# Kernel tuning notes

Hardware: AMD Instinct MI355X
Metric: run time of the kernel (lower is better)

Reference implementation:

```python
import jax, jax.numpy as jnp
import numpy as np

N_NODES = 10000
N_EDGES = 320000
D = 128
H = 4
C = 128
L = 2
NEG_SLOPE = 0.2
LN_EPS = 1e-5


def setup_inputs() -> dict:
    key = jax.random.key(0)
    ks = jax.random.split(key, 8)
    x = jax.random.normal(ks[0], (N_NODES, D), dtype=jnp.float32)
    edge_index = jax.random.randint(ks[1], (2, N_EDGES), 0, N_NODES, dtype=jnp.int64)
    # weights scaled ~Glorot to keep attention logits in a sane range
    Wl = jax.random.normal(ks[2], (L, D, H * C), dtype=jnp.float32) * 0.1
    Wr = jax.random.normal(ks[3], (L, D, H * C), dtype=jnp.float32) * 0.1
    att = jax.random.normal(ks[4], (L, H, C), dtype=jnp.float32) * 0.1
    return {
        "x": x,
        "edge_index": edge_index,
        "Wl": Wl,
        "bl": jnp.zeros((L, H * C), jnp.float32),
        "Wr": Wr,
        "br": jnp.zeros((L, H * C), jnp.float32),
        "att": att,
        "bias": jnp.zeros((L, D), jnp.float32),
        "ln_g": jnp.ones((L, D), jnp.float32),
        "ln_b": jnp.zeros((L, D), jnp.float32),
    }


def _gatv2_layer(x, src, dst, Wl, bl, Wr, br, att, b):
    """GATv2Conv (concat=False -> head mean), messages src->dst, softmax over dst."""
    n = x.shape[0]
    xl = (x @ Wl + bl).reshape(n, H, C)  # source transform
    xr = (x @ Wr + br).reshape(n, H, C)  # target transform
    s = jax.nn.leaky_relu(xl[src] + xr[dst], NEG_SLOPE)  # [E, H, C]
    e = jnp.einsum("ehc,hc->eh", s, att)  # attention logits [E, H]
    m = jax.ops.segment_max(e, dst, num_segments=n)  # stable softmax per dst segment
    ex = jnp.exp(e - m[dst])
    denom = jax.ops.segment_sum(ex, dst, num_segments=n)
    alpha = ex / denom[dst]  # [E, H]
    out = jax.ops.segment_sum(alpha[:, :, None] * xl[src], dst, num_segments=n)  # [N, H, C]
    return out.mean(axis=1) + b  # concat=False -> mean over heads, then bias


def _layer_norm(h, g, b):
    mu = h.mean(-1, keepdims=True)
    var = ((h - mu) ** 2).mean(-1, keepdims=True)
    return (h - mu) * jax.lax.rsqrt(var + LN_EPS) * g + b


def reference(x, edge_index, Wl, bl, Wr, br, att, bias, ln_g, ln_b):
    n = x.shape[0]
    loop = jnp.arange(n, dtype=edge_index.dtype)
    src = jnp.concatenate([edge_index[0], loop])  # add self-loops (PyG default)
    dst = jnp.concatenate([edge_index[1], loop])
    for i in range(L):
        h = _gatv2_layer(x, src, dst, Wl[i], bl[i], Wr[i], br[i], att[i], bias[i])
        x = h + x  # residual
        x = jax.nn.relu(_layer_norm(x, ln_g[i], ln_b[i]))
    return x
```

## Files before the change

kernel.cpp:

```cpp
#include <hip/hip_runtime.h>
#include <math.h>

#define N_NODES 10000
#define N_EDGES 320000
#define E_TOT   (N_EDGES + N_NODES)
#define NEG 0.2f
#define CAP 96

typedef short bf16x8 __attribute__((ext_vector_type(8)));
typedef float f32x4 __attribute__((ext_vector_type(4)));
typedef float f32x2 __attribute__((ext_vector_type(2)));

static __device__ __forceinline__ float4 ld4g(const float* p) { return *(const float4*)p; }

static __device__ __forceinline__ uint4 ldg4(const unsigned short* p, unsigned byteoff) {
    return *(const uint4*)((const char*)p + byteoff);
}

static __device__ __forceinline__ unsigned short f2b(float f) {
    unsigned u;
    __builtin_memcpy(&u, &f, 4);
    unsigned r = (u + 0x7fffu + ((u >> 16) & 1u)) >> 16;
    return (unsigned short)r;
}
static __device__ __forceinline__ f32x2 unpk(unsigned d) {
    f32x2 r;
    r.x = __uint_as_float(d << 16);
    r.y = __uint_as_float(d & 0xffff0000u);
    return r;
}

template <int CTRL>
static __device__ __forceinline__ float dpp_add_step(float x) {
    int y = __builtin_amdgcn_update_dpp(0, __float_as_int(x), CTRL, 0xf, 0xf, true);
    return x + __int_as_float(y);
}
static __device__ __forceinline__ float row_sum16(float x) {
    x = dpp_add_step<0x121>(x);
    x = dpp_add_step<0x122>(x);
    x = dpp_add_step<0x124>(x);
    x = dpp_add_step<0x128>(x);
    return x;
}

__global__ __launch_bounds__(256) void prep_fused_kernel(
    const float* __restrict__ x,
    const float* __restrict__ Wl, const float* __restrict__ Wr,
    unsigned short* __restrict__ xb, unsigned short* __restrict__ WT,
    int* __restrict__ deg) {
    int tid = threadIdx.x, bid = blockIdx.x;
    __shared__ float tbuf[32][33];

    for (int i = bid * 256 + tid; i < N_NODES; i += 256 * 256) deg[i] = 0;

    int l = bid >> 7;
    int rest = bid & 127;
    int ky = rest >> 5, nx = rest & 31;
    int n0 = nx * 32, k0 = ky * 32;
    const float* S = ((n0 < 512) ? Wl : Wr) + (size_t)l * 65536;
    int nn0 = n0 & 511;
    int tx = tid & 31, ty = tid >> 5;
#pragma unroll
    for (int it = 0; it < 4; ++it) {
        int k = k0 + ty + it * 8;
        tbuf[ty + it * 8][tx] = S[(size_t)k * 512 + nn0 + tx];
    }
    __syncthreads();
    unsigned short* dstp = WT + (size_t)l * 1024 * 128;
#pragma unroll
    for (int it = 0; it < 4; ++it) {
        int n = n0 + ty + it * 8;
        int k = k0 + tx;
        dstp[(size_t)n * 128 + k] = f2b(tbuf[tx][ty + it * 8]);
    }
    for (int i = bid * 256 + tid; i < N_NODES * 32; i += 256 * 256) {
        float4 v = ld4g(x + 4 * i);
        ushort4 o = make_ushort4(f2b(v.x), f2b(v.y), f2b(v.z), f2b(v.w));
        *(ushort4*)(xb + 4 * i) = o;
    }
}

template <int DO_FILL>
__global__ __launch_bounds__(256) void gemm_mfma_kernel(const unsigned short* __restrict__ A,
                                                        const unsigned short* __restrict__ Bt,
                                                        const float* __restrict__ bl,
                                                        const float* __restrict__ br,
                                                        unsigned short* __restrict__ Y,
                                                        const int* __restrict__ ei,
                                                        int* __restrict__ deg,
                                                        int* __restrict__ csr_src) {
    __shared__ unsigned short As[128][72];
    __shared__ unsigned short Bs[128][72];
    int tid = threadIdx.x;
    int wave = tid >> 6, lane = tid & 63;
    int wm = wave >> 1, wn = wave & 1;
    int l15 = lane & 15, quad = lane >> 4;
    int row0 = blockIdx.y * 128, col0 = blockIdx.x * 128;
    const float* bias = (col0 < 512) ? (bl + col0) : (br + col0 - 512);

    f32x4 acc[4][4];
#pragma unroll
    for (int mi = 0; mi < 4; ++mi)
#pragma unroll
        for (int ni = 0; ni < 4; ++ni)
#pragma unroll
            for (int r = 0; r < 4; ++r) acc[mi][ni][r] = 0.f;

#pragma unroll
    for (int kc = 0; kc < 2; ++kc) {
#pragma unroll
        for (int it = 0; it < 4; ++it) {
            int e = tid + it * 256;
            int r = e >> 3, s = e & 7;
            int gr = row0 + r;
            bf16x8 v = (bf16x8)(short)0;
            if (gr < N_NODES) v = *(const bf16x8*)(A + (size_t)gr * 128 + kc * 64 + s * 8);
            *(bf16x8*)&As[r][s * 8] = v;
            bf16x8 w = *(const bf16x8*)(Bt + (size_t)(col0 + r) * 128 + kc * 64 + s * 8);
            *(bf16x8*)&Bs[r][s * 8] = w;
        }
        __syncthreads();
#pragma unroll
        for (int kq = 0; kq < 2; ++kq) {
            bf16x8 af[4], bfr[4];
#pragma unroll
            for (int mi = 0; mi < 4; ++mi)
                af[mi] = *(const bf16x8*)&As[wm * 64 + mi * 16 + l15][kq * 32 + quad * 8];
#pragma unroll
            for (int ni = 0; ni < 4; ++ni)
                bfr[ni] = *(const bf16x8*)&Bs[wn * 64 + ni * 16 + l15][kq * 32 + quad * 8];
#pragma unroll
            for (int mi = 0; mi < 4; ++mi)
#pragma unroll
                for (int ni = 0; ni < 4; ++ni)
                    acc[mi][ni] = __builtin_amdgcn_mfma_f32_16x16x32_bf16(af[mi], bfr[ni], acc[mi][ni], 0, 0, 0);
        }
        __syncthreads();
    }

    float bv[4];
#pragma unroll
    for (int ni = 0; ni < 4; ++ni) bv[ni] = bias[wn * 64 + ni * 16 + l15];

#pragma unroll
    for (int mi = 0; mi < 4; ++mi) {
#pragma unroll
        for (int r = 0; r < 4; ++r) {
            int grow = row0 + wm * 64 + mi * 16 + quad * 4 + r;
            if (grow >= N_NODES) continue;
#pragma unroll
            for (int ni = 0; ni < 4; ++ni) {
                int gcol = col0 + wn * 64 + ni * 16 + l15;
                Y[(size_t)grow * 1024 + gcol] = f2b(acc[mi][ni][r] + bv[ni]);
            }
        }
    }

    if (DO_FILL) {
        bool is64 = ((ei[1] | ei[3] | ei[5] | ei[7]) == 0);
        int nthreads = gridDim.x * gridDim.y * 256;
        int gid = (blockIdx.y * gridDim.x + blockIdx.x) * 256 + tid;
        for (int i = gid; i < E_TOT; i += nthreads) {
            int src, dst;
            if (i < N_EDGES) {
                if (is64) { const long long* e = (const long long*)ei; src = (int)e[i]; dst = (int)e[N_EDGES + i]; }
                else { src = ei[i]; dst = ei[N_EDGES + i]; }
            } else {
                src = dst = i - N_EDGES;
            }
            int pos = atomicAdd(&deg[dst], 1);
            if (pos < CAP) csr_src[dst * CAP + pos] = src;
        }
    }
}

__global__ __launch_bounds__(256) void attn_kernel(
    const unsigned short* __restrict__ xlr,
    const float* __restrict__ x_in, const int* __restrict__ deg,
    const int* __restrict__ csr_src, const float* __restrict__ att,
    const float* __restrict__ bias, const float* __restrict__ ln_g,
    const float* __restrict__ ln_b, float* __restrict__ x_out,
    unsigned short* __restrict__ xb_out) {
    int wv = (blockIdx.x * blockDim.x + threadIdx.x) >> 6;
    if (wv >= N_NODES) return;
    int lane = threadIdx.x & 63;
    int dst = __builtin_amdgcn_readfirstlane(wv);
    int g = lane & 15;
    int off = 8 * lane;
    unsigned boff = (unsigned)off << 1;

    f32x2 xr2[4], at2[4];
    {
        const unsigned short* xrrow = xlr + ((size_t)(unsigned)dst << 10) + 512;
        uint4 u = ldg4(xrrow, boff);
        xr2[0] = unpk(u.x); xr2[1] = unpk(u.y); xr2[2] = unpk(u.z); xr2[3] = unpk(u.w);
        float4 a = ld4g(att + off);
        float4 b = ld4g(att + off + 4);
        at2[0].x = a.x; at2[0].y = a.y; at2[1].x = a.z; at2[1].y = a.w;
        at2[2].x = b.x; at2[2].y = b.y; at2[3].x = b.z; at2[3].y = b.w;
    }
    const f32x2 neg2 = {NEG, NEG};

    float d = 0.f;
    f32x2 acc2[4] = {{0.f, 0.f}, {0.f, 0.f}, {0.f, 0.f}, {0.f, 0.f}};

    int len = deg[dst];
    if (len > CAP) len = CAP;
    const int* cp = csr_src + dst * CAP;
    int nfull = len & ~3;
    int p = 0;

    if (nfull) {
        int4 I = *(const int4*)cp;
        {
            const unsigned short* r0 = xlr + ((size_t)(unsigned)I.x << 10);
            const unsigned short* r1 = xlr + ((size_t)(unsigned)I.y << 10);
            const unsigned short* r2 = xlr + ((size_t)(unsigned)I.z << 10);
            const unsigned short* r3 = xlr + ((size_t)(unsigned)I.w << 10);
            uint4 u0 = ldg4(r0, boff);
            uint4 u1 = ldg4(r1, boff);
            uint4 u2 = ldg4(r2, boff);
            uint4 u3 = ldg4(r3, boff);
            if (4 < nfull) I = *(const int4*)(cp + 4);
            while (true) {
                p += 4;
                bool more = p < nfull;
                uint4 n0, n1, n2, n3;
                if (more) {
                    const unsigned short* q0 = xlr + ((size_t)(unsigned)I.x << 10);
                    const unsigned short* q1 = xlr + ((size_t)(unsigned)I.y << 10);
                    const unsigned short* q2 = xlr + ((size_t)(unsigned)I.z << 10);
                    const unsigned short* q3 = xlr + ((size_t)(unsigned)I.w << 10);
                    n0 = ldg4(q0, boff);
                    n1 = ldg4(q1, boff);
                    n2 = ldg4(q2, boff);
                    n3 = ldg4(q3, boff);
                    if (p + 4 < nfull) I = *(const int4*)(cp + p + 4);
                }
                f32x2 F0[4], F1[4], F2[4], F3[4];
                {
                    const unsigned* w0 = (const unsigned*)&u0;
                    const unsigned* w1 = (const unsigned*)&u1;
                    const unsigned* w2 = (const unsigned*)&u2;
                    const unsigned* w3 = (const unsigned*)&u3;
#pragma unroll
                    for (int q = 0; q < 4; ++q) {
                        F0[q] = unpk(w0[q]); F1[q] = unpk(w1[q]);
                        F2[q] = unpk(w2[q]); F3[q] = unpk(w3[q]);
                    }
                }
                f32x2 q0 = {0.f, 0.f}, q1 = {0.f, 0.f}, q2 = {0.f, 0.f}, q3 = {0.f, 0.f};
#pragma unroll
                for (int q = 0; q < 4; ++q) {
                    f32x2 s;
                    s = F0[q] + xr2[q]; s = __builtin_elementwise_max(s, s * neg2);
                    q0 = __builtin_elementwise_fma(s, at2[q], q0);
                    s = F1[q] + xr2[q]; s = __builtin_elementwise_max(s, s * neg2);
                    q1 = __builtin_elementwise_fma(s, at2[q], q1);
                    s = F2[q] + xr2[q]; s = __builtin_elementwise_max(s, s * neg2);
                    q2 = __builtin_elementwise_fma(s, at2[q], q2);
                    s = F3[q] + xr2[q]; s = __builtin_elementwise_max(s, s * neg2);
                    q3 = __builtin_elementwise_fma(s, at2[q], q3);
                }
                float p0 = row_sum16(q0.x + q0.y);
                float p1 = row_sum16(q1.x + q1.y);
                float p2 = row_sum16(q2.x + q2.y);
                float p3 = row_sum16(q3.x + q3.y);
                float e0 = __expf(p0), e1 = __expf(p1), e2 = __expf(p2), e3 = __expf(p3);
                d += (e0 + e1) + (e2 + e3);
                f32x2 W0 = {e0, e0}, W1 = {e1, e1}, W2 = {e2, e2}, W3 = {e3, e3};
#pragma unroll
                for (int q = 0; q < 4; ++q) {
                    f32x2 t = __builtin_elementwise_fma(F0[q], W0, acc2[q]);
                    t = __builtin_elementwise_fma(F1[q], W1, t);
                    t = __builtin_elementwise_fma(F2[q], W2, t);
                    acc2[q] = __builtin_elementwise_fma(F3[q], W3, t);
                }
                if (!more) break;
                u0 = n0; u1 = n1; u2 = n2; u3 = n3;
            }
        }
    }
    for (; p < len; ++p) {
        int s0 = cp[p];
        const unsigned short* rp = xlr + ((size_t)(unsigned)s0 << 10);
        uint4 u0 = ldg4(rp, boff);
        const unsigned* w0 = (const unsigned*)&u0;
        f32x2 F0[4];
#pragma unroll
        for (int q = 0; q < 4; ++q) F0[q] = unpk(w0[q]);
        f32x2 q0 = {0.f, 0.f};
#pragma unroll
        for (int q = 0; q < 4; ++q) {
            f32x2 s = F0[q] + xr2[q];
            s = __builtin_elementwise_max(s, s * neg2);
            q0 = __builtin_elementwise_fma(s, at2[q], q0);
        }
        float p0 = row_sum16(q0.x + q0.y);
        float e0 = __expf(p0);
        d += e0;
        f32x2 W0 = {e0, e0};
#pragma unroll
        for (int q = 0; q < 4; ++q)
            acc2[q] = __builtin_elementwise_fma(F0[q], W0, acc2[q]);
    }

    float inv = 1.f / d;
    float t[8];
#pragma unroll
    for (int q = 0; q < 4; ++q) {
        t[2 * q] = acc2[q].x * inv;
        t[2 * q + 1] = acc2[q].y * inv;
    }
#pragma unroll
    for (int j = 0; j < 8; ++j) {
        t[j] += __shfl_xor(t[j], 16, 64);
        t[j] += __shfl_xor(t[j], 32, 64);
    }
    float4 bi0 = ld4g(bias + 8 * g), bi1 = ld4g(bias + 8 * g + 4);
    float4 xi0 = ld4g(x_in + (size_t)dst * 128 + 8 * g);
    float4 xi1 = ld4g(x_in + (size_t)dst * 128 + 8 * g + 4);
    float hc[8];
    hc[0] = t[0] * 0.25f + bi0.x + xi0.x;
    hc[1] = t[1] * 0.25f + bi0.y + xi0.y;
    hc[2] = t[2] * 0.25f + bi0.z + xi0.z;
    hc[3] = t[3] * 0.25f + bi0.w + xi0.w;
    hc[4] = t[4] * 0.25f + bi1.x + xi1.x;
    hc[5] = t[5] * 0.25f + bi1.y + xi1.y;
    hc[6] = t[6] * 0.25f + bi1.z + xi1.z;
    hc[7] = t[7] * 0.25f + bi1.w + xi1.w;

    float sm = 0.f, sq = 0.f;
#pragma unroll
    for (int j = 0; j < 8; ++j) { sm += hc[j]; sq = fmaf(hc[j], hc[j], sq); }
    sm = row_sum16(sm);
    sq = row_sum16(sq);
    float mu = sm * (1.f / 128.f);
    float var = sq * (1.f / 128.f) - mu * mu;
    float rs = rsqrtf(var + 1e-5f);
    float4 g0 = ld4g(ln_g + 8 * g), g1 = ld4g(ln_g + 8 * g + 4);
    float4 b0 = ld4g(ln_b + 8 * g), b1 = ld4g(ln_b + 8 * g + 4);
    float y[8];
    y[0] = fmaxf((hc[0] - mu) * rs * g0.x + b0.x, 0.f);
    y[1] = fmaxf((hc[1] - mu) * rs * g0.y + b0.y, 0.f);
    y[2] = fmaxf((hc[2] - mu) * rs * g0.z + b0.z, 0.f);
    y[3] = fmaxf((hc[3] - mu) * rs * g0.w + b0.w, 0.f);
    y[4] = fmaxf((hc[4] - mu) * rs * g1.x + b1.x, 0.f);
    y[5] = fmaxf((hc[5] - mu) * rs * g1.y + b1.y, 0.f);
    y[6] = fmaxf((hc[6] - mu) * rs * g1.z + b1.z, 0.f);
    y[7] = fmaxf((hc[7] - mu) * rs * g1.w + b1.w, 0.f);

    if (lane < 16) {
        float4 o0 = make_float4(y[0], y[1], y[2], y[3]);
        float4 o1 = make_float4(y[4], y[5], y[6], y[7]);
        *(float4*)(x_out + (size_t)dst * 128 + 8 * g) = o0;
        *(float4*)(x_out + (size_t)dst * 128 + 8 * g + 4) = o1;
        if (xb_out) {
            ushort4 c0 = make_ushort4(f2b(y[0]), f2b(y[1]), f2b(y[2]), f2b(y[3]));
            ushort4 c1 = make_ushort4(f2b(y[4]), f2b(y[5]), f2b(y[6]), f2b(y[7]));
            *(ushort4*)(xb_out + (size_t)dst * 128 + 8 * g) = c0;
            *(ushort4*)(xb_out + (size_t)dst * 128 + 8 * g + 4) = c1;
        }
    }
}

extern "C" void kernel_launch(void* const* d_in, const int* in_sizes, int n_in,
                              void* d_out, int out_size, void* d_ws, size_t ws_size,
                              hipStream_t stream) {
    const float* x    = (const float*)d_in[0];
    const int*   ei   = (const int*)d_in[1];
    const float* Wl   = (const float*)d_in[2];
    const float* bl   = (const float*)d_in[3];
    const float* Wr   = (const float*)d_in[4];
    const float* br   = (const float*)d_in[5];
    const float* att  = (const float*)d_in[6];
    const float* bias = (const float*)d_in[7];
    const float* lng  = (const float*)d_in[8];
    const float* lnb  = (const float*)d_in[9];
    float* out = (float*)d_out;

    char* ws = (char*)d_ws;
    unsigned short* xlr = (unsigned short*)ws; ws += (size_t)N_NODES * 1024 * 2;
    float* xbuf  = (float*)ws;          ws += (size_t)N_NODES * 128 * 4;
    unsigned short* xb = (unsigned short*)ws; ws += (size_t)N_NODES * 128 * 2;
    unsigned short* WT = (unsigned short*)ws; ws += (size_t)2 * 1024 * 128 * 2;
    int* deg     = (int*)ws;            ws += (size_t)N_NODES * 4;
    int* csr_src = (int*)ws;            ws += (size_t)N_NODES * CAP * 4;

    prep_fused_kernel<<<256, 256, 0, stream>>>(x, Wl, Wr, xb, WT, deg);

    for (int l = 0; l < 2; ++l) {
        const float* xin = (l == 0) ? x : xbuf;
        float* xout = (l == 0) ? xbuf : out;
        unsigned short* xbo = (l == 0) ? xb : (unsigned short*)nullptr;
        if (l == 0)
            gemm_mfma_kernel<1><<<dim3(8, 79), 256, 0, stream>>>(
                xb, WT, bl, br, xlr, ei, deg, csr_src);
        else
            gemm_mfma_kernel<0><<<dim3(8, 79), 256, 0, stream>>>(
                xb, WT + (size_t)1024 * 128, bl + 512, br + 512, xlr, ei, deg, csr_src);
        attn_kernel<<<(N_NODES * 64 + 255) / 256, 256, 0, stream>>>(
            xlr, xin, deg, csr_src,
            att + (size_t)l * 512, bias + (size_t)l * 128,
            lng + (size_t)l * 128, lnb + (size_t)l * 128, xout, xbo);
    }
}
```

Baseline: 208.0 us.

## Split attention per head with head-major layout and separate combine kernel

The GEMM output moves to head-major planes (xl and xr stored per head), and the attention kernel now gives each wave one (head, dst) pair, with the four lanes-groups taking different edges. Block indices are swizzled so heads of the same dst chunk run close together. Per-head results go to an fp32 hpart buffer, and a new combine kernel does the head mean, residual, LayerNorm and ReLU. The aim is better gather locality and parallelism per head, at the cost of an extra kernel launch per layer, extra hpart traffic, and four times as many waves reading each index list.

Result: slower. 214.2 us (+2.9%).

```diff
diff --git a/kernel.cpp b/kernel.cpp
--- a/kernel.cpp
+++ b/kernel.cpp
@@ -16,6 +16,7 @@
 static __device__ __forceinline__ uint4 ldg4(const unsigned short* p, unsigned byteoff) {
     return *(const uint4*)((const char*)p + byteoff);
 }
+static __device__ __forceinline__ int ldgi(const int* p, int e) { return p[e]; }
 
 static __device__ __forceinline__ unsigned short f2b(float f) {
     unsigned u;
@@ -41,6 +42,32 @@
     x = dpp_add_step<0x124>(x);
     x = dpp_add_step<0x128>(x);
     return x;
+}
+
+static __device__ __forceinline__ void comp_round(
+    uint4 u, bool valid,
+    const f32x2* __restrict__ xr2, const f32x2* __restrict__ at2,
+    f32x2* __restrict__ acc2, float* __restrict__ dsum) {
+    const f32x2 neg2 = {NEG, NEG};
+    const unsigned* w = (const unsigned*)&u;
+    f32x2 F[4];
+#pragma unroll
+    for (int q = 0; q < 4; ++q) F[q] = unpk(w[q]);
+    f32x2 qq = {0.f, 0.f};
+#pragma unroll
+    for (int q = 0; q < 4; ++q) {
+        f32x2 s = F[q] + xr2[q];
+        s = __builtin_elementwise_max(s, s * neg2);
+        qq = __builtin_elementwise_fma(s, at2[q], qq);
+    }
+    float qs = row_sum16(qq.x + qq.y);
+    float ev = __expf(qs);
+    ev = valid ? ev : 0.f;
+    *dsum += ev;
+    f32x2 W = {ev, ev};
+#pragma unroll
+    for (int q = 0; q < 4; ++q)
+        acc2[q] = __builtin_elementwise_fma(F[q], W, acc2[q]);
 }
 
 __global__ __launch_bounds__(256) void prep_fused_kernel(
@@ -85,7 +112,8 @@
                                                         const unsigned short* __restrict__ Bt,
                                                         const float* __restrict__ bl,
                                                         const float* __restrict__ br,
-                                                        unsigned short* __restrict__ Y,
+                                                        unsigned short* __restrict__ xlh,
+                                                        unsigned short* __restrict__ xrh,
                                                         const int* __restrict__ ei,
                                                         int* __restrict__ deg,
                                                         int* __restrict__ csr_src) {
@@ -142,6 +170,9 @@
 #pragma unroll
     for (int ni = 0; ni < 4; ++ni) bv[ni] = bias[wn * 64 + ni * 16 + l15];
 
+    int h = (col0 >> 7) & 3;
+    unsigned short* dstb = ((col0 < 512) ? xlh : xrh) + (((size_t)h * N_NODES) << 7);
+
 #pragma unroll
     for (int mi = 0; mi < 4; ++mi) {
 #pragma unroll
@@ -150,8 +181,8 @@
             if (grow >= N_NODES) continue;
 #pragma unroll
             for (int ni = 0; ni < 4; ++ni) {
-                int gcol = col0 + wn * 64 + ni * 16 + l15;
-                Y[(size_t)grow * 1024 + gcol] = f2b(acc[mi][ni][r] + bv[ni]);
+                int cc = wn * 64 + ni * 16 + l15;
+                dstb[((size_t)grow << 7) + cc] = f2b(acc[mi][ni][r] + bv[ni]);
             }
         }
     }
@@ -175,9 +206,90 @@
 }
 
 __global__ __launch_bounds__(256) void attn_kernel(
-    const unsigned short* __restrict__ xlr,
-    const float* __restrict__ x_in, const int* __restrict__ deg,
-    const int* __restrict__ csr_src, const float* __restrict__ att,
+    const unsigned short* __restrict__ xlh,
+    const unsigned short* __restrict__ xrh,
+    const int* __restrict__ deg, const int* __restrict__ csr_src,
+    const float* __restrict__ att,
+    float* __restrict__ hpart) {
+    int tid = threadIdx.x;
+    unsigned bid = blockIdx.x;
+    int w = tid >> 6, lane = tid & 63;
+    int head = (int)((bid & 7u) >> 1);
+    int chunk = (int)((bid >> 3) * 2 + (bid & 1u));
+    int dst = chunk * 4 + w;
+    head = __builtin_amdgcn_readfirstlane(head);
+    dst = __builtin_amdgcn_readfirstlane(dst);
+    int e = lane >> 4, g = lane & 15;
+    unsigned gboff = (unsigned)(g << 4);
+
+    const unsigned short* XL = xlh + (((size_t)head * N_NODES) << 7);
+
+    f32x2 xr2[4], at2[4];
+    {
+        const unsigned short* xrrow = xrh + (((size_t)head * N_NODES + (size_t)dst) << 7);
+        uint4 u = *(const uint4*)(xrrow + g * 8);
+        xr2[0] = unpk(u.x); xr2[1] = unpk(u.y); xr2[2] = unpk(u.z); xr2[3] = unpk(u.w);
+        const float* ap = att + head * 128 + g * 8;
+        float4 a = ld4g(ap);
+        float4 b = ld4g(ap + 4);
+        at2[0].x = a.x; at2[0].y = a.y; at2[1].x = a.z; at2[1].y = a.w;
+        at2[2].x = b.x; at2[2].y = b.y; at2[3].x = b.z; at2[3].y = b.w;
+    }
+
+    float d = 0.f;
+    f32x2 acc2[4] = {{0.f, 0.f}, {0.f, 0.f}, {0.f, 0.f}, {0.f, 0.f}};
+
+    int len = deg[dst];
+    if (len > CAP) len = CAP;
+    const int* cp = csr_src + dst * CAP;
+    int rounds = (len + 3) >> 2;
+
+    int i1 = (rounds > 1) ? ldgi(cp + 4, e) : 0;
+    int i2 = (rounds > 2) ? ldgi(cp + 8, e) : 0;
+    int ic0 = (e < len) ? ldgi(cp, e) : 0;
+    {
+        int raw = ldgi(cp, e);
+        ic0 = (e < len) ? raw : 0;
+    }
+    uint4 uc = ldg4(XL, ((unsigned)ic0 << 8) + gboff);
+    uint4 un = uc;
+
+    for (int r = 0; r < rounds; ++r) {
+        bool more = (r + 1) < rounds;
+        if (more) {
+            int vm = len - 4 * (r + 1);
+            int icn = (e < vm) ? i1 : 0;
+            un = ldg4(XL, ((unsigned)icn << 8) + gboff);
+            i1 = i2;
+            i2 = ((r + 3) < rounds) ? ldgi(cp + 4 * (r + 3), e) : 0;
+        }
+        comp_round(uc, e < (len - 4 * r), xr2, at2, acc2, &d);
+        uc = un;
+    }
+
+    float t[8];
+#pragma unroll
+    for (int q = 0; q < 4; ++q) { t[2 * q] = acc2[q].x; t[2 * q + 1] = acc2[q].y; }
+#pragma unroll
+    for (int j = 0; j < 8; ++j) {
+        t[j] += __shfl_xor(t[j], 16, 64);
+        t[j] += __shfl_xor(t[j], 32, 64);
+    }
+    d += __shfl_xor(d, 16, 64);
+    d += __shfl_xor(d, 32, 64);
+    float inv = 1.f / d;
+#pragma unroll
+    for (int j = 0; j < 8; ++j) t[j] *= inv;
+
+    if (lane < 16) {
+        float* op = hpart + (((size_t)head * N_NODES + (size_t)dst) << 7) + g * 8;
+        *(float4*)op = make_float4(t[0], t[1], t[2], t[3]);
+        *(float4*)(op + 4) = make_float4(t[4], t[5], t[6], t[7]);
+    }
+}
+
+__global__ __launch_bounds__(256) void combine_kernel(
+    const float* __restrict__ hpart, const float* __restrict__ x_in,
     const float* __restrict__ bias, const float* __restrict__ ln_g,
     const float* __restrict__ ln_b, float* __restrict__ x_out,
     unsigned short* __restrict__ xb_out) {
@@ -185,182 +297,32 @@
     if (wv >= N_NODES) return;
     int lane = threadIdx.x & 63;
     int dst = __builtin_amdgcn_readfirstlane(wv);
-    int g = lane & 15;
-    int off = 8 * lane;
-    unsigned boff = (unsigned)off << 1;
-
-    f32x2 xr2[4], at2[4];
-    {
-        const unsigned short* xrrow = xlr + ((size_t)(unsigned)dst << 10) + 512;
-        uint4 u = ldg4(xrrow, boff);
-        xr2[0] = unpk(u.x); xr2[1] = unpk(u.y); xr2[2] = unpk(u.z); xr2[3] = unpk(u.w);
-        float4 a = ld4g(att + off);
-        float4 b = ld4g(att + off + 4);
-        at2[0].x = a.x; at2[0].y = a.y; at2[1].x = a.z; at2[1].y = a.w;
-        at2[2].x = b.x; at2[2].y = b.y; at2[3].x = b.z; at2[3].y = b.w;
-    }
-    const f32x2 neg2 = {NEG, NEG};
-
-    float d = 0.f;
-    f32x2 acc2[4] = {{0.f, 0.f}, {0.f, 0.f}, {0.f, 0.f}, {0.f, 0.f}};
-
-    int len = deg[dst];
-    if (len > CAP) len = CAP;
-    const int* cp = csr_src + dst * CAP;
-    int nfull = len & ~3;
-    int p = 0;
-
-    if (nfull) {
-        int4 I = *(const int4*)cp;
-        {
-            const unsigned short* r0 = xlr + ((size_t)(unsigned)I.x << 10);
-            const unsigned short* r1 = xlr + ((size_t)(unsigned)I.y << 10);
-            const unsigned short* r2 = xlr + ((size_t)(unsigned)I.z << 10);
-            const unsigned short* r3 = xlr + ((size_t)(unsigned)I.w << 10);
-            uint4 u0 = ldg4(r0, boff);
-            uint4 u1 = ldg4(r1, boff);
-            uint4 u2 = ldg4(r2, boff);
-            uint4 u3 = ldg4(r3, boff);
-            if (4 < nfull) I = *(const int4*)(cp + 4);
-            while (true) {
-                p += 4;
-                bool more = p < nfull;
-                uint4 n0, n1, n2, n3;
-                if (more) {
-                    const unsigned short* q0 = xlr + ((size_t)(unsigned)I.x << 10);
-                    const unsigned short* q1 = xlr + ((size_t)(unsigned)I.y << 10);
-                    const unsigned short* q2 = xlr + ((size_t)(unsigned)I.z << 10);
-                    const unsigned short* q3 = xlr + ((size_t)(unsigned)I.w << 10);
-                    n0 = ldg4(q0, boff);
-                    n1 = ldg4(q1, boff);
-                    n2 = ldg4(q2, boff);
-                    n3 = ldg4(q3, boff);
-                    if (p + 4 < nfull) I = *(const int4*)(cp + p + 4);
-                }
-                f32x2 F0[4], F1[4], F2[4], F3[4];
-                {
-                    const unsigned* w0 = (const unsigned*)&u0;
-                    const unsigned* w1 = (const unsigned*)&u1;
-                    const unsigned* w2 = (const unsigned*)&u2;
-                    const unsigned* w3 = (const unsigned*)&u3;
-#pragma unroll
-                    for (int q = 0; q < 4; ++q) {
-                        F0[q] = unpk(w0[q]); F1[q] = unpk(w1[q]);
-                        F2[q] = unpk(w2[q]); F3[q] = unpk(w3[q]);
-                    }
-                }
-                f32x2 q0 = {0.f, 0.f}, q1 = {0.f, 0.f}, q2 = {0.f, 0.f}, q3 = {0.f, 0.f};
-#pragma unroll
-                for (int q = 0; q < 4; ++q) {
-                    f32x2 s;
-                    s = F0[q] + xr2[q]; s = __builtin_elementwise_max(s, s * neg2);
-                    q0 = __builtin_elementwise_fma(s, at2[q], q0);
-                    s = F1[q] + xr2[q]; s = __builtin_elementwise_max(s, s * neg2);
-                    q1 = __builtin_elementwise_fma(s, at2[q], q1);
-                    s = F2[q] + xr2[q]; s = __builtin_elementwise_max(s, s * neg2);
-                    q2 = __builtin_elementwise_fma(s, at2[q], q2);
-                    s = F3[q] + xr2[q]; s = __builtin_elementwise_max(s, s * neg2);
-                    q3 = __builtin_elementwise_fma(s, at2[q], q3);
-                }
-                float p0 = row_sum16(q0.x + q0.y);
-                float p1 = row_sum16(q1.x + q1.y);
-                float p2 = row_sum16(q2.x + q2.y);
-                float p3 = row_sum16(q3.x + q3.y);
-                float e0 = __expf(p0), e1 = __expf(p1), e2 = __expf(p2), e3 = __expf(p3);
-                d += (e0 + e1) + (e2 + e3);
-                f32x2 W0 = {e0, e0}, W1 = {e1, e1}, W2 = {e2, e2}, W3 = {e3, e3};
-#pragma unroll
-                for (int q = 0; q < 4; ++q) {
-                    f32x2 t = __builtin_elementwise_fma(F0[q], W0, acc2[q]);
-                    t = __builtin_elementwise_fma(F1[q], W1, t);
-                    t = __builtin_elementwise_fma(F2[q], W2, t);
-                    acc2[q] = __builtin_elementwise_fma(F3[q], W3, t);
-                }
-                if (!more) break;
-                u0 = n0; u1 = n1; u2 = n2; u3 = n3;
-            }
-        }
-    }
-    for (; p < len; ++p) {
-        int s0 = cp[p];
-        const unsigned short* rp = xlr + ((size_t)(unsigned)s0 << 10);
-        uint4 u0 = ldg4(rp, boff);
-        const unsigned* w0 = (const unsigned*)&u0;
-        f32x2 F0[4];
-#pragma unroll
-        for (int q = 0; q < 4; ++q) F0[q] = unpk(w0[q]);
-        f32x2 q0 = {0.f, 0.f};
-#pragma unroll
-        for (int q = 0; q < 4; ++q) {
-            f32x2 s = F0[q] + xr2[q];
-            s = __builtin_elementwise_max(s, s * neg2);
-            q0 = __builtin_elementwise_fma(s, at2[q], q0);
-        }
-        float p0 = row_sum16(q0.x + q0.y);
-        float e0 = __expf(p0);
-        d += e0;
-        f32x2 W0 = {e0, e0};
-#pragma unroll
-        for (int q = 0; q < 4; ++q)
-            acc2[q] = __builtin_elementwise_fma(F0[q], W0, acc2[q]);
-    }
-
-    float inv = 1.f / d;
-    float t[8];
-#pragma unroll
-    for (int q = 0; q < 4; ++q) {
-        t[2 * q] = acc2[q].x * inv;
-        t[2 * q + 1] = acc2[q].y * inv;
-    }
-#pragma unroll
-    for (int j = 0; j < 8; ++j) {
-        t[j] += __shfl_xor(t[j], 16, 64);
-        t[j] += __shfl_xor(t[j], 32, 64);
-    }
-    float4 bi0 = ld4g(bias + 8 * g), bi1 = ld4g(bias + 8 * g + 4);
-    float4 xi0 = ld4g(x_in + (size_t)dst * 128 + 8 * g);
-    float4 xi1 = ld4g(x_in + (size_t)dst * 128 + 8 * g + 4);
-    float hc[8];
-    hc[0] = t[0] * 0.25f + bi0.x + xi0.x;
-    hc[1] = t[1] * 0.25f + bi0.y + xi0.y;
-    hc[2] = t[2] * 0.25f + bi0.z + xi0.z;
-    hc[3] = t[3] * 0.25f + bi0.w + xi0.w;
-    hc[4] = t[4] * 0.25f + bi1.x + xi1.x;
-    hc[5] = t[5] * 0.25f + bi1.y + xi1.y;
-    hc[6] = t[6] * 0.25f + bi1.z + xi1.z;
-    hc[7] = t[7] * 0.25f + bi1.w + xi1.w;
-
-    float sm = 0.f, sq = 0.f;
-#pragma unroll
-    for (int j = 0; j < 8; ++j) { sm += hc[j]; sq = fmaf(hc[j], hc[j], sq); }
-    sm = row_sum16(sm);
-    sq = row_sum16(sq);
+    int c = lane * 2;
+    const float* hp = hpart + ((size_t)dst << 7) + c;
+    const size_t hs = ((size_t)N_NODES) << 7;
+    f32x2 h0 = *(const f32x2*)(hp);
+    f32x2 h1 = *(const f32x2*)(hp + hs);
+    f32x2 h2 = *(const f32x2*)(hp + 2 * hs);
+    f32x2 h3 = *(const f32x2*)(hp + 3 * hs);
+    f32x2 bi = *(const f32x2*)(bias + c);
+    f32x2 xi = *(const f32x2*)(x_in + ((size_t)dst << 7) + c);
+    f32x2 hc = ((h0 + h1) + (h2 + h3)) * 0.25f + bi + xi;
+    float sm = hc.x + hc.y;
+    float sq = hc.x * hc.x + hc.y * hc.y;
+    sm = row_sum16(sm); sm += __shfl_xor(sm, 16, 64); sm += __shfl_xor(sm, 32, 64);
+    sq = row_sum16(sq); sq += __shfl_xor(sq, 16, 64); sq += __shfl_xor(sq, 32, 64);
     float mu = sm * (1.f / 128.f);
     float var = sq * (1.f / 128.f) - mu * mu;
     float rs = rsqrtf(var + 1e-5f);
-    float4 g0 = ld4g(ln_g + 8 * g), g1 = ld4g(ln_g + 8 * g + 4);
-    float4 b0 = ld4g(ln_b + 8 * g), b1 = ld4g(ln_b + 8 * g + 4);
-    float y[8];
-    y[0] = fmaxf((hc[0] - mu) * rs * g0.x + b0.x, 0.f);
-    y[1] = fmaxf((hc[1] - mu) * rs * g0.y + b0.y, 0.f);
-    y[2] = fmaxf((hc[2] - mu) * rs * g0.z + b0.z, 0.f);
-    y[3] = fmaxf((hc[3] - mu) * rs * g0.w + b0.w, 0.f);
-    y[4] = fmaxf((hc[4] - mu) * rs * g1.x + b1.x, 0.f);
-    y[5] = fmaxf((hc[5] - mu) * rs * g1.y + b1.y, 0.f);
-    y[6] = fmaxf((hc[6] - mu) * rs * g1.z + b1.z, 0.f);
-    y[7] = fmaxf((hc[7] - mu) * rs * g1.w + b1.w, 0.f);
-
-    if (lane < 16) {
-        float4 o0 = make_float4(y[0], y[1], y[2], y[3]);
-        float4 o1 = make_float4(y[4], y[5], y[6], y[7]);
-        *(float4*)(x_out + (size_t)dst * 128 + 8 * g) = o0;
-        *(float4*)(x_out + (size_t)dst * 128 + 8 * g + 4) = o1;
-        if (xb_out) {
-            ushort4 c0 = make_ushort4(f2b(y[0]), f2b(y[1]), f2b(y[2]), f2b(y[3]));
-            ushort4 c1 = make_ushort4(f2b(y[4]), f2b(y[5]), f2b(y[6]), f2b(y[7]));
-            *(ushort4*)(xb_out + (size_t)dst * 128 + 8 * g) = c0;
-            *(ushort4*)(xb_out + (size_t)dst * 128 + 8 * g + 4) = c1;
-        }
+    f32x2 gg = *(const f32x2*)(ln_g + c);
+    f32x2 bb = *(const f32x2*)(ln_b + c);
+    float y0 = fmaxf((hc.x - mu) * rs * gg.x + bb.x, 0.f);
+    float y1 = fmaxf((hc.y - mu) * rs * gg.y + bb.y, 0.f);
+    f32x2 y = {y0, y1};
+    *(f32x2*)(x_out + ((size_t)dst << 7) + c) = y;
+    if (xb_out) {
+        unsigned pk = ((unsigned)f2b(y0)) | (((unsigned)f2b(y1)) << 16);
+        *(unsigned*)(xb_out + ((size_t)dst << 7) + c) = pk;
     }
 }
 
@@ -380,7 +342,9 @@
     float* out = (float*)d_out;
 
     char* ws = (char*)d_ws;
-    unsigned short* xlr = (unsigned short*)ws; ws += (size_t)N_NODES * 1024 * 2;
+    unsigned short* xlh = (unsigned short*)ws; ws += (size_t)4 * N_NODES * 128 * 2;
+    unsigned short* xrh = (unsigned short*)ws; ws += (size_t)4 * N_NODES * 128 * 2;
+    float* hpart = (float*)ws;          ws += (size_t)4 * N_NODES * 128 * 4;
     float* xbuf  = (float*)ws;          ws += (size_t)N_NODES * 128 * 4;
     unsigned short* xb = (unsigned short*)ws; ws += (size_t)N_NODES * 128 * 2;
     unsigned short* WT = (unsigned short*)ws; ws += (size_t)2 * 1024 * 128 * 2;
@@ -395,13 +359,14 @@
         unsigned short* xbo = (l == 0) ? xb : (unsigned short*)nullptr;
         if (l == 0)
             gemm_mfma_kernel<1><<<dim3(8, 79), 256, 0, stream>>>(
-                xb, WT, bl, br, xlr, ei, deg, csr_src);
+                xb, WT, bl, br, xlh, xrh, ei, deg, csr_src);
         else
             gemm_mfma_kernel<0><<<dim3(8, 79), 256, 0, stream>>>(
-                xb, WT + (size_t)1024 * 128, bl + 512, br + 512, xlr, ei, deg, csr_src);
-        attn_kernel<<<(N_NODES * 64 + 255) / 256, 256, 0, stream>>>(
-            xlr, xin, deg, csr_src,
-            att + (size_t)l * 512, bias + (size_t)l * 128,
+                xb, WT + (size_t)1024 * 128, bl + 512, br + 512, xlh, xrh, ei, deg, csr_src);
+        attn_kernel<<<10000, 256, 0, stream>>>(
+            xlh, xrh, deg, csr_src, att + (size_t)l * 512, hpart);
+        combine_kernel<<<2500, 256, 0, stream>>>(
+            hpart, xin, bias + (size_t)l * 128,
             lng + (size_t)l * 128, lnb + (size_t)l * 128, xout, xbo);
     }
 }
```
